# Performance work log

Measured on AMD Instinct MI355X. Metric: run time of the kernel, lower is better.

Reference implementation:

```python
import jax, jax.numpy as jnp
import numpy as np

T, B, K = 512, 1024, 48            # time steps, batch, tagset size
START, STOP = K - 2, K - 1         # tag_to_ix[START_TAG], tag_to_ix[STOP_TAG]
NEG = -10000.0


def setup_inputs() -> dict:
    key = jax.random.key(0)
    k1, k2, k3, k4 = jax.random.split(key, 4)
    # post-tanh emission features (output of tanh(hidden2tag(...))), time-major [T,B,K]
    feats = jnp.tanh(jax.random.normal(k1, (T, B, K), dtype=jnp.float32))
    transitions = jax.random.normal(k2, (K, K), dtype=jnp.float32)
    # CRF structural constraints, same as torch init:
    transitions = transitions.at[START, :].set(NEG).at[:, STOP].set(NEG)
    tags = jax.random.randint(k3, (B, T), 0, K - 2)       # gold tags exclude START/STOP
    lengths = jax.random.randint(k4, (B,), 1, T + 1)      # valid sequence lengths
    return {"feats": feats, "transitions": transitions, "tags": tags, "lengths": lengths}


def _crf_loss(feats, transitions, tags, lengths):
    Tn, Bn, Kn = feats.shape
    mask = jnp.arange(Tn)[:, None] < lengths[None, :]            # [T,B] valid-token mask

    # ---- forward algorithm (logZ) ----
    alpha0 = jnp.full((Bn, Kn), NEG, dtype=feats.dtype).at[:, START].set(0.0)

    def step(alpha, x):
        feat_t, m_t = x                                          # [B,K], [B]
        # scores[b, next, prev] = alpha[b,prev] + trans[next,prev] + emit[b,next]
        scores = alpha[:, None, :] + transitions[None, :, :] + feat_t[:, :, None]
        new_alpha = jax.nn.logsumexp(scores, axis=2)             # [B,K]
        alpha = jnp.where(m_t[:, None], new_alpha, alpha)        # freeze finished seqs
        return alpha, None

    alpha, _ = jax.lax.scan(step, alpha0, (feats, mask))
    log_z = jax.nn.logsumexp(alpha + transitions[STOP][None, :], axis=1)  # [B]

    # ---- gold path score ----
    tags_ext = jnp.concatenate(
        [jnp.full((Bn, 1), START, dtype=tags.dtype), tags], axis=1)       # [B,T+1]
    prev_t = tags_ext[:, :-1]                                             # [B,T]
    next_t = tags_ext[:, 1:]                                              # [B,T]
    feats_bt = feats.transpose(1, 0, 2)                                   # [B,T,K]
    emit = jnp.take_along_axis(feats_bt, next_t[:, :, None], axis=2)[:, :, 0]  # [B,T]
    trans_s = transitions[next_t, prev_t]                                 # [B,T]
    gold = jnp.sum(jnp.where(mask.T, trans_s + emit, 0.0), axis=1)        # [B]
    last_tag = jnp.take_along_axis(tags_ext, lengths[:, None], axis=1)[:, 0]
    gold = gold + transitions[STOP, last_tag]

    return jnp.sum(log_z - gold)


def reference(feats, transitions, tags, lengths):
    return _crf_loss(feats, transitions, tags, lengths)
```

## Files before the change

### kernel.cpp

```cpp
#include <hip/hip_runtime.h>
#include <math.h>

#define T_LEN 512
#define B_N   1024
#define K_N   48
#define START_TAG (K_N - 2)
#define STOP_TAG  (K_N - 1)
#define NEG   -10000.0f


__device__ __forceinline__ float bcast(float v, int k) {
    return __uint_as_float(__builtin_amdgcn_readlane(__float_as_uint(v), k));
}

__device__ __forceinline__ float matvec48(const float (&E)[48], float src) {
    float a0 = 0.f, a1 = 0.f, a2 = 0.f, a3 = 0.f;
    #pragma unroll
    for (int k = 0; k < 48; k += 4) {
        a0 = fmaf(E[k + 0], bcast(src, k + 0), a0);
        a1 = fmaf(E[k + 1], bcast(src, k + 1), a1);
        a2 = fmaf(E[k + 2], bcast(src, k + 2), a2);
        a3 = fmaf(E[k + 3], bcast(src, k + 3), a3);
    }
    return (a0 + a1) + (a2 + a3);
}

__device__ __forceinline__ void renorm(float& q, float& C) {
    const float g = bcast(q, 0);
    C += __logf(g);
    q *= __builtin_amdgcn_rcpf(g);
}

template <int BWD>
__device__ __forceinline__ void run_chain(const float* __restrict__ fb,
                                          const float (&E)[48],
                                          int steps, int lm1, int lane_c,
                                          float& q, float& C)
{
    const size_t sT = (size_t)B_N * K_N;
    auto row_of = [&](int i) -> int {
        int r = BWD ? (lm1 - i) : i;
        r = (r < 0) ? 0 : r;
        r = (r > lm1) ? lm1 : r;
        return r;
    };
    auto step = [&](int t, float fv) {
        const bool on = t < steps;
        if (BWD) {
            const float u = q * __expf(fv);
            const float w = matvec48(E, u);
            q = on ? w : q;
        } else {
            const float w = matvec48(E, q);
            q = on ? w * __expf(fv) : q;
        }
    };

    float f0[8], f1[8];
    #pragma unroll
    for (int i = 0; i < 8; ++i)
        f0[i] = fb[(size_t)row_of(i) * sT + lane_c];

    const int nblk = (steps + 15) >> 4;
    #pragma unroll 1
    for (int blk = 0; blk < nblk; ++blk) {
        const int t0 = blk * 16;
        #pragma unroll
        for (int i = 0; i < 8; ++i)
            f1[i] = fb[(size_t)row_of(t0 + 8 + i) * sT + lane_c];
        #pragma unroll
        for (int i = 0; i < 8; ++i) {
            step(t0 + i, f0[i]);
            if (i == 3 || i == 7) renorm(q, C);
        }
        #pragma unroll
        for (int i = 0; i < 8; ++i)
            f0[i] = fb[(size_t)row_of(t0 + 16 + i) * sT + lane_c];
        #pragma unroll
        for (int i = 0; i < 8; ++i) {
            step(t0 + 8 + i, f1[i]);
            if (i == 3 || i == 7) renorm(q, C);
        }
    }
}

__global__ __launch_bounds__(1024)
void lpt_sort_kernel(const int* __restrict__ lengths, int* __restrict__ perm)
{
    __shared__ int hist[512];
    __shared__ int offs[512];
    const int tid = threadIdx.x;
    if (tid < 512) hist[tid] = 0;
    __syncthreads();
    const int len = lengths[tid];
    const int key = 512 - len;
    atomicAdd(&hist[key], 1);
    __syncthreads();
    if (tid < 512) offs[tid] = hist[tid];
    __syncthreads();
    for (int d = 1; d < 512; d <<= 1) {
        int v = 0;
        if (tid < 512 && tid >= d) v = offs[tid - d];
        __syncthreads();
        if (tid < 512) offs[tid] += v;
        __syncthreads();
    }
    const int p = atomicSub(&offs[key], 1) - 1;
    perm[p] = tid;
}

__global__ __launch_bounds__(128)
__attribute__((amdgpu_waves_per_eu(1, 1)))
void crf_fused_kernel(
    const float* __restrict__ feats,
    const float* __restrict__ trans,
    const int*   __restrict__ tags,
    const int*   __restrict__ lengths,
    const int*   __restrict__ perm,
    float* __restrict__ out)
{
    const int b      = perm[blockIdx.x];
    const int tid    = threadIdx.x;
    const int lane   = tid & 63;
    const int wid    = tid >> 6;
    const int len    = lengths[b];
    const int lm1    = len - 1;
    const int m      = (len + 1) >> 1;
    const int steps  = wid ? (len - m) : m;
    const int lane_c = (lane < K_N) ? lane : (K_N - 1);

    __shared__ __attribute__((aligned(16))) float sh_p[64];
    __shared__ float sh_cb;
    __shared__ float sh_gold;

    float E[48];
    if (wid == 0) {
        const float* tr = trans + lane_c * K_N;
        #pragma unroll
        for (int k = 0; k < 48; ++k) E[k] = __expf(tr[k]);
    } else {
        #pragma unroll
        for (int k = 0; k < 48; ++k) E[k] = __expf(trans[k * K_N + lane_c]);
    }

    const float* fb = feats + (size_t)b * K_N;
    const size_t sT = (size_t)B_N * K_N;

    float q, C = 0.0f;
    if (wid == 0) q = (lane == START_TAG) ? 1.0f : 0.0f;
    else          q = __expf(trans[STOP_TAG * K_N + lane_c]);

    if (wid == 0) run_chain<0>(fb, E, steps, lm1, lane_c, q, C);
    else          run_chain<1>(fb, E, steps, lm1, lane_c, q, C);
    renorm(q, C);

    if (wid == 1) {
        float gsum = 0.0f;
        for (int t = lane; t < len; t += 64) {
            int next = tags[(size_t)b * T_LEN + t];
            int prev = (t == 0) ? START_TAG : tags[(size_t)b * T_LEN + t - 1];
            gsum += trans[next * K_N + prev] + fb[(size_t)t * sT + next];
        }
        #pragma unroll
        for (int off = 32; off >= 1; off >>= 1)
            gsum += __shfl_xor(gsum, off);

        sh_p[lane] = q;
        if (lane == 0) {
            sh_cb = C;
            int last = tags[(size_t)b * T_LEN + len - 1];
            sh_gold = gsum + trans[STOP_TAG * K_N + last];
        }
    }
    __syncthreads();

    if (wid == 0) {
        float term = (lane < K_N) ? q * sh_p[lane] : 0.0f;
        #pragma unroll
        for (int off = 32; off >= 1; off >>= 1)
            term += __shfl_xor(term, off);
        if (lane == 0) {
            float log_z = C + sh_cb + __logf(term);
            atomicAdd(out, log_z - sh_gold);
        }
    }
}

extern "C" void kernel_launch(void* const* d_in, const int* in_sizes, int n_in,
                              void* d_out, int out_size, void* d_ws, size_t ws_size,
                              hipStream_t stream) {
    const float* feats   = (const float*)d_in[0];
    const float* trans   = (const float*)d_in[1];
    const int*   tags    = (const int*)d_in[2];
    const int*   lengths = (const int*)d_in[3];
    float* out = (float*)d_out;
    int*   perm = (int*)d_ws;

    hipMemsetAsync(out, 0, sizeof(float) * out_size, stream);
    lpt_sort_kernel<<<1, B_N, 0, stream>>>(lengths, perm);
    crf_fused_kernel<<<B_N, 128, 0, stream>>>(feats, trans, tags, lengths, perm, out);
}
```

Measured before the change: 195.4 us.

## Use packed FMA with SGPR-pair broadcast, skip START/STOP columns, peel first step

```diff
diff --git a/kernel.cpp b/kernel.cpp
--- a/kernel.cpp
+++ b/kernel.cpp
@@ -9,20 +9,29 @@
 #define NEG   -10000.0f
 
 
+using f32x2 = __attribute__((ext_vector_type(2))) float;
+
 __device__ __forceinline__ float bcast(float v, int k) {
     return __uint_as_float(__builtin_amdgcn_readlane(__float_as_uint(v), k));
 }
 
-__device__ __forceinline__ float matvec48(const float (&E)[48], float src) {
-    float a0 = 0.f, a1 = 0.f, a2 = 0.f, a3 = 0.f;
-    #pragma unroll
-    for (int k = 0; k < 48; k += 4) {
-        a0 = fmaf(E[k + 0], bcast(src, k + 0), a0);
-        a1 = fmaf(E[k + 1], bcast(src, k + 1), a1);
-        a2 = fmaf(E[k + 2], bcast(src, k + 2), a2);
-        a3 = fmaf(E[k + 3], bcast(src, k + 3), a3);
-    }
-    return (a0 + a1) + (a2 + a3);
+__device__ __forceinline__ float matvec46(const f32x2 (&E2)[23], float src) {
+    const int qb = __float_as_int(src);
+    f32x2 a0 = {0.f, 0.f}, a1 = {0.f, 0.f}, a2 = {0.f, 0.f}, a3 = {0.f, 0.f};
+#define PKFMA(P, ACC) { \
+        const unsigned int lo = (unsigned int)__builtin_amdgcn_readlane(qb, 2*(P)); \
+        const unsigned int hi = (unsigned int)__builtin_amdgcn_readlane(qb, 2*(P)+1); \
+        const unsigned long long sp = ((unsigned long long)hi << 32) | lo; \
+        asm("v_pk_fma_f32 %0, %1, %2, %0" : "+v"(ACC) : "v"(E2[P]), "s"(sp)); }
+    PKFMA(0,a0)  PKFMA(1,a1)  PKFMA(2,a2)  PKFMA(3,a3)
+    PKFMA(4,a0)  PKFMA(5,a1)  PKFMA(6,a2)  PKFMA(7,a3)
+    PKFMA(8,a0)  PKFMA(9,a1)  PKFMA(10,a2) PKFMA(11,a3)
+    PKFMA(12,a0) PKFMA(13,a1) PKFMA(14,a2) PKFMA(15,a3)
+    PKFMA(16,a0) PKFMA(17,a1) PKFMA(18,a2) PKFMA(19,a3)
+    PKFMA(20,a0) PKFMA(21,a1) PKFMA(22,a2)
+#undef PKFMA
+    const f32x2 s = (a0 + a1) + (a2 + a3);
+    return s.x + s.y;
 }
 
 __device__ __forceinline__ void renorm(float& q, float& C) {
@@ -33,25 +42,25 @@
 
 template <int BWD>
 __device__ __forceinline__ void run_chain(const float* __restrict__ fb,
-                                          const float (&E)[48],
-                                          int steps, int lm1, int lane_c,
+                                          int rbase,
+                                          const f32x2 (&E2)[23],
+                                          int steps, int lane_c,
                                           float& q, float& C)
 {
     const size_t sT = (size_t)B_N * K_N;
     auto row_of = [&](int i) -> int {
-        int r = BWD ? (lm1 - i) : i;
+        int r = BWD ? (rbase - i) : (rbase + i);
         r = (r < 0) ? 0 : r;
-        r = (r > lm1) ? lm1 : r;
+        r = (r > T_LEN - 1) ? (T_LEN - 1) : r;
         return r;
     };
-    auto step = [&](int t, float fv) {
-        const bool on = t < steps;
+    auto step = [&](bool on, float fv) {
         if (BWD) {
             const float u = q * __expf(fv);
-            const float w = matvec48(E, u);
+            const float w = matvec46(E2, u);
             q = on ? w : q;
         } else {
-            const float w = matvec48(E, q);
+            const float w = matvec46(E2, q);
             q = on ? w * __expf(fv) : q;
         }
     };
@@ -61,16 +70,16 @@
     for (int i = 0; i < 8; ++i)
         f0[i] = fb[(size_t)row_of(i) * sT + lane_c];
 
-    const int nblk = (steps + 15) >> 4;
+    const int nfull = steps >> 4;
     #pragma unroll 1
-    for (int blk = 0; blk < nblk; ++blk) {
+    for (int blk = 0; blk < nfull; ++blk) {
         const int t0 = blk * 16;
         #pragma unroll
         for (int i = 0; i < 8; ++i)
             f1[i] = fb[(size_t)row_of(t0 + 8 + i) * sT + lane_c];
         #pragma unroll
         for (int i = 0; i < 8; ++i) {
-            step(t0 + i, f0[i]);
+            step(true, f0[i]);
             if (i == 3 || i == 7) renorm(q, C);
         }
         #pragma unroll
@@ -78,7 +87,24 @@
             f0[i] = fb[(size_t)row_of(t0 + 16 + i) * sT + lane_c];
         #pragma unroll
         for (int i = 0; i < 8; ++i) {
-            step(t0 + 8 + i, f1[i]);
+            step(true, f1[i]);
+            if (i == 3 || i == 7) renorm(q, C);
+        }
+    }
+    const int rem = steps & 15;
+    if (rem) {
+        const int t0 = nfull * 16;
+        #pragma unroll
+        for (int i = 0; i < 8; ++i)
+            f1[i] = fb[(size_t)row_of(t0 + 8 + i) * sT + lane_c];
+        #pragma unroll
+        for (int i = 0; i < 8; ++i) {
+            step(i < rem, f0[i]);
+            if (i == 3 || i == 7) renorm(q, C);
+        }
+        #pragma unroll
+        for (int i = 0; i < 8; ++i) {
+            step(8 + i < rem, f1[i]);
             if (i == 3 || i == 7) renorm(q, C);
         }
     }
@@ -126,32 +152,42 @@
     const int len    = lengths[b];
     const int lm1    = len - 1;
     const int m      = (len + 1) >> 1;
-    const int steps  = wid ? (len - m) : m;
     const int lane_c = (lane < K_N) ? lane : (K_N - 1);
 
     __shared__ __attribute__((aligned(16))) float sh_p[64];
     __shared__ float sh_cb;
     __shared__ float sh_gold;
 
-    float E[48];
+    const float* fb = feats + (size_t)b * K_N;
+    const size_t sT = (size_t)B_N * K_N;
+
+    f32x2 E2[23];
     if (wid == 0) {
         const float* tr = trans + lane_c * K_N;
         #pragma unroll
-        for (int k = 0; k < 48; ++k) E[k] = __expf(tr[k]);
+        for (int p = 0; p < 23; ++p) {
+            E2[p].x = __expf(tr[2 * p]);
+            E2[p].y = __expf(tr[2 * p + 1]);
+        }
     } else {
         #pragma unroll
-        for (int k = 0; k < 48; ++k) E[k] = __expf(trans[k * K_N + lane_c]);
-    }
-
-    const float* fb = feats + (size_t)b * K_N;
-    const size_t sT = (size_t)B_N * K_N;
+        for (int p = 0; p < 23; ++p) {
+            E2[p].x = __expf(trans[(2 * p) * K_N + lane_c]);
+            E2[p].y = __expf(trans[(2 * p + 1) * K_N + lane_c]);
+        }
+    }
 
     float q, C = 0.0f;
-    if (wid == 0) q = (lane == START_TAG) ? 1.0f : 0.0f;
-    else          q = __expf(trans[STOP_TAG * K_N + lane_c]);
-
-    if (wid == 0) run_chain<0>(fb, E, steps, lm1, lane_c, q, C);
-    else          run_chain<1>(fb, E, steps, lm1, lane_c, q, C);
+    int   steps;
+    if (wid == 0) {
+        q = __expf(trans[lane_c * K_N + START_TAG] + fb[lane_c]);
+        steps = m - 1;
+        run_chain<0>(fb, 1, E2, steps, lane_c, q, C);
+    } else {
+        q = __expf(trans[STOP_TAG * K_N + lane_c]);
+        steps = len - m;
+        run_chain<1>(fb, lm1, E2, steps, lane_c, q, C);
+    }
     renorm(q, C);
 
     if (wid == 1) {
```

New measurement: 192.2 us. About the same (-1.7%).
